# Kernel optimization log

Measured on AMD Instinct MI355X. Metric: run time of the kernel, lower is better.

Reference implementation:

```python
import jax, jax.numpy as jnp
import numpy as np
import math

NEG = -1e9


def maximum_path(neg_cent, text_len, spec_len):
    # neg_cent: [B, Ts, Tt]; monotonic alignment (Viterbi) DP as in VITS.
    B, Ts, Tt = neg_cent.shape
    jj = jnp.arange(Tt)
    tt = jnp.arange(Ts)
    node_mask = (jj[None, None, :] < text_len[:, None, None]) & (tt[None, :, None] < spec_len[:, None, None])
    nc = jnp.where(node_mask, neg_cent, NEG)

    def fstep(q, nc_t):
        # q: [B, Tt] best score ending at text index j at previous frame
        q_shift = jnp.concatenate([jnp.full((B, 1), NEG, q.dtype), q[:, :-1]], axis=1)
        d = q_shift >= q  # True -> came from j-1 (diagonal move)
        q_new = nc_t + jnp.maximum(q, q_shift)
        return q_new, d

    q0 = jnp.broadcast_to(jnp.where(jj == 0, 0.0, NEG), (B, Tt)).astype(neg_cent.dtype)
    _, dirs = jax.lax.scan(fstep, q0, jnp.swapaxes(nc, 0, 1))  # dirs: [Ts, B, Tt]

    def bstep(j, inp):
        t, d_t = inp
        start = (t == spec_len - 1)
        j_eff = jnp.where(start, text_len - 1, j)
        valid = t < spec_len
        emit = ((jj[None, :] == j_eff[:, None]) & valid[:, None]).astype(neg_cent.dtype)
        came_diag = jnp.take_along_axis(d_t, j_eff[:, None], axis=1)[:, 0]
        j_next = jnp.where(valid, jnp.maximum(j_eff - came_diag.astype(j_eff.dtype), 0), j_eff)
        return j_next, emit

    j_init = jnp.zeros((B,), text_len.dtype)
    _, path = jax.lax.scan(bstep, j_init, (jnp.arange(Ts), dirs), reverse=True)
    return jnp.swapaxes(path, 0, 1)  # [B, Ts, Tt]


def setup_inputs() -> dict:
    B, C, Ts, Tt = 16, 192, 2048, 512
    key = jax.random.key(0)
    k1, k2, k3, k4, k5 = jax.random.split(key, 5)
    z_p = jax.random.normal(k1, (B, C, Ts), dtype=jnp.float32)
    m_p = jax.random.normal(k2, (B, C, Tt), dtype=jnp.float32)
    logs_p = 0.1 * jax.random.normal(k3, (B, C, Tt), dtype=jnp.float32)
    text_len = jax.random.randint(k4, (B,), Tt // 2, Tt + 1, dtype=jnp.int32)
    extra = jax.random.randint(k5, (B,), 0, Ts - Tt + 1, dtype=jnp.int32)
    spec_len = jnp.minimum(text_len + extra, Ts)
    return {"z_p": z_p, "m_p": m_p, "logs_p": logs_p, "spec_len": spec_len, "text_len": text_len}


def reference(z_p, m_p, logs_p, spec_len, text_len):
    B, C, Ts = z_p.shape
    Tt = m_p.shape[2]
    text_mask = (jnp.arange(Tt)[None, :] < text_len[:, None]).astype(z_p.dtype)[:, None, :]  # [B,1,Tt]
    spec_mask = (jnp.arange(Ts)[None, :] < spec_len[:, None]).astype(z_p.dtype)[:, None, :]  # [B,1,Ts]

    # --- neg_cent (torch.no_grad block) ---
    s_p_sq_r = jnp.exp(-2.0 * logs_p)  # [B,C,Tt]
    neg_cent1 = jnp.sum(-0.5 * math.log(2.0 * math.pi) - logs_p, axis=1, keepdims=True)  # [B,1,Tt]
    neg_cent2 = jnp.einsum('bct,bcu->btu', -0.5 * z_p ** 2, s_p_sq_r)  # [B,Ts,Tt]
    neg_cent3 = jnp.einsum('bct,bcu->btu', z_p, m_p * s_p_sq_r)  # [B,Ts,Tt]
    neg_cent4 = jnp.sum(-0.5 * m_p ** 2 * s_p_sq_r, axis=1, keepdims=True)  # [B,1,Tt]
    neg_cent = neg_cent1 + neg_cent2 + neg_cent3 + neg_cent4

    path = jax.lax.stop_gradient(maximum_path(neg_cent, text_len, spec_len))  # [B,Ts,Tt]

    duration = jnp.sum(path, axis=1)[:, None, :]  # [B,1,Tt]
    logw_ = jnp.log(duration + 1e-6) * text_mask  # [B,1,Tt]

    # expand prior stats along the alignment path: [B,C,Ts]
    m_p_exp = jnp.einsum('btu,bcu->bct', path, m_p)
    logs_p_exp = jnp.einsum('btu,bcu->bct', path, logs_p)

    return (path, duration, logw_, m_p_exp, logs_p_exp, text_mask, spec_mask)
```

## Files before the change

kernel.cpp:

```cpp
#include <hip/hip_runtime.h>
#include <hip/hip_bf16.h>
#include <math.h>

#define BB 16
#define CC 192
#define TS 2048
#define TT 512
#define KK 384

#define OFF_PATH 0
#define OFF_DUR  (16777216)
#define OFF_LOGW (OFF_DUR + 8192)
#define OFF_MEXP (OFF_LOGW + 8192)
#define OFF_LEXP (OFF_MEXP + 6291456)
#define OFF_TMASK (OFF_LEXP + 6291456)
#define OFF_SMASK (OFF_TMASK + 8192)

#define NEGCF (-1e9f)

__global__ __launch_bounds__(512) void vits_prep(
    const float* __restrict__ m_p, const float* __restrict__ logs_p,
    const int* __restrict__ spec_len, const int* __restrict__ text_len,
    float* __restrict__ Bmat, float* __restrict__ avec,
    float* __restrict__ tmask, float* __restrict__ smask)
{
    const int b = blockIdx.x;
    const int u = threadIdx.x;
    const float C0 = -0.91893853320467274178f;
    float a_acc = 0.f;
    for (int c = 0; c < CC; ++c) {
        float lg = logs_p[((size_t)b*CC + c)*TT + u];
        float mm = m_p[((size_t)b*CC + c)*TT + u];
        float s  = expf(-2.f*lg);
        float ms = mm * s;
        Bmat[((size_t)b*KK + 2*c    )*TT + u] = ms;
        Bmat[((size_t)b*KK + 2*c + 1)*TT + u] = s;
        a_acc += C0 - lg - 0.5f*mm*ms;
    }
    avec[b*TT + u] = a_acc;
    tmask[b*TT + u] = (u < text_len[b]) ? 1.f : 0.f;
    for (int t = u; t < TS; t += TT)
        smask[b*TS + t] = (t < spec_len[b]) ? 1.f : 0.f;
}

__global__ __launch_bounds__(256) void vits_gemm(
    const float* __restrict__ z, const float* __restrict__ Bmat,
    const float* __restrict__ avec, float* __restrict__ out)
{
    const int b  = blockIdx.z;
    const int t0 = blockIdx.y * 64;
    const int u0 = blockIdx.x * 64;
    __shared__ float As[16][68];
    __shared__ float Bs[16][68];
    const int tid = threadIdx.x;
    const int tx = tid & 15, ty = tid >> 4;
    float acc[4][4] = {};
    const float* zb = z    + (size_t)b * CC * TS;
    const float* Bb = Bmat + (size_t)b * KK * TT;
    for (int kc = 0; kc < KK/16; ++kc) {
        {
            int c_l = tid >> 5;
            int t_l = (tid & 31) * 2;
            const float* zp = zb + (size_t)(kc*8 + c_l)*TS + t0 + t_l;
            float2 zv = *(const float2*)zp;
            float2 z1 = make_float2(zv.x, zv.y);
            float2 z2 = make_float2(-0.5f*zv.x*zv.x, -0.5f*zv.y*zv.y);
            *(float2*)&As[2*c_l  ][t_l] = z1;
            *(float2*)&As[2*c_l+1][t_l] = z2;
            int k_l = tid >> 4;
            int u_l = (tid & 15) * 4;
            const float* bp = Bb + (size_t)(kc*16 + k_l)*TT + u0 + u_l;
            *(float4*)&Bs[k_l][u_l] = *(const float4*)bp;
        }
        __syncthreads();
        #pragma unroll
        for (int kk = 0; kk < 16; ++kk) {
            float4 av = *(const float4*)&As[kk][ty*4];
            float4 bv = *(const float4*)&Bs[kk][tx*4];
            float aa[4] = {av.x, av.y, av.z, av.w};
            float bb[4] = {bv.x, bv.y, bv.z, bv.w};
            #pragma unroll
            for (int i = 0; i < 4; ++i)
                #pragma unroll
                for (int jj = 0; jj < 4; ++jj)
                    acc[i][jj] += aa[i]*bb[jj];
        }
        __syncthreads();
    }
    float4 a4 = *(const float4*)(avec + b*TT + u0 + tx*4);
    float ab[4] = {a4.x, a4.y, a4.z, a4.w};
    #pragma unroll
    for (int i = 0; i < 4; ++i) {
        float4 o;
        o.x = acc[i][0] + ab[0];
        o.y = acc[i][1] + ab[1];
        o.z = acc[i][2] + ab[2];
        o.w = acc[i][3] + ab[3];
        *(float4*)(out + ((size_t)b*TS + t0 + ty*4 + i)*TT + u0 + tx*4) = o;
    }
}

__device__ __forceinline__ float dpp_ror1_f32(float v) {
    union { float f; int i; } u, r;
    u.f = v;
    r.i = __builtin_amdgcn_update_dpp(0, u.i, 0x13C, 0xF, 0xF, false);
    return r.f;
}

#define DIRS(j,w) dirs[((j)<<6) | ((w) ^ ((j) & 31))]
#define RING 16

__global__ __launch_bounds__(1024, 1) void vits_dp(
    const float* __restrict__ nc,
    const int* __restrict__ spec_len, const int* __restrict__ text_len,
    float* __restrict__ dur, float* __restrict__ logw, int* __restrict__ jt)
{
    __shared__ unsigned int dirs[TT*(TS/32)];
    __shared__ float qrow[TT];
    __shared__ int Tr[TT + 1];

    const int tid  = threadIdx.x;
    const int lane = tid & 63;
    const int wid  = tid >> 6;
    const int b = blockIdx.x;
    const int SL = spec_len[b], TL = text_len[b];
    const int col = (wid << 5) + lane - 32;
    const bool auth = (lane >= 32);
    const bool w0g  = (wid == 0) && (lane < 32);

    float q = (col == 0) ? 0.0f : NEGCF;
    unsigned int bits = 0;

    const int colL = (col < 0) ? 0 : col;
    const float* ncb = nc + (size_t)b*TS*TT + colL;

    float pf[RING];
    #pragma unroll
    for (int i = 0; i < RING; ++i) pf[i] = ncb[(size_t)i*TT];
    const float* pcur = ncb + (size_t)RING*TT;

    int tb = 0;
    for (; tb + 32 <= SL; tb += 32) {
        #pragma unroll
        for (int s = 0; s < 32; ++s) {
            const int t = tb + s;
            float f = pf[s & (RING-1)];
            pf[s & (RING-1)] = *pcur;
            pcur += TT;

            float qp = dpp_ror1_f32(q);
            bool d = (qp >= q);
            bits = (bits << 1) | (unsigned)d;
            float qn = f + fmaxf(qp, q);
            q = w0g ? NEGCF : qn;

            if (s == 31) {
                int w = t >> 5;
                if (auth) {
                    DIRS(col, w) = bits;
                    qrow[col] = q;
                }
                bits = 0;
                __syncthreads();
                if (!auth && wid != 0) q = qrow[col];
                __syncthreads();
            }
        }
    }
    for (int t = tb; t < SL; ++t) {
        float f = ncb[(size_t)t*TT];
        float qp = dpp_ror1_f32(q);
        bool d = (qp >= q);
        bits = (bits << 1) | (unsigned)d;
        float qn = f + fmaxf(qp, q);
        q = w0g ? NEGCF : qn;
    }
    if (SL & 31) {
        int w = SL >> 5, r = SL & 31;
        if (auth) DIRS(col, w) = bits << (32 - r);
    }
    __syncthreads();

    for (int i = tid; i <= TT; i += 1024) Tr[i] = 0;
    __syncthreads();

    if (tid == 0) {
        Tr[TL] = SL;
        int j = TL - 1, tc = SL - 1;
        while (j > 0 && tc >= 0) {
            int w = tc >> 5;
            int bcur = 31 - (tc & 31);
            unsigned int W = DIRS(j, w) & (0xFFFFFFFFu << bcur);
            if (W) {
                int bp = __ffs(W) - 1;
                int tp = (w << 5) + 31 - bp;
                Tr[j] = tp;
                --j;
                tc = tp - 1;
            } else {
                if (w == 0) break;
                tc = (w << 5) - 1;
            }
        }
    }
    __syncthreads();

    for (int u = tid; u < TT; u += 1024) {
        float dv = (u < TL) ? (float)(Tr[u+1] - Tr[u]) : 0.0f;
        dur[b*TT + u] = dv;
        logw[b*TT + u] = (u < TL) ? logf(dv + 1e-6f) : 0.0f;
    }
    for (int u = 0; u < TL; ++u) {
        int t1 = Tr[u+1];
        for (int t = Tr[u] + tid; t < t1; t += 1024) jt[b*TS + t] = u;
    }
    for (int t = SL + tid; t < TS; t += 1024) jt[b*TS + t] = -1;
}

__global__ void vits_path(const int* __restrict__ jt, float4* __restrict__ path)
{
    int idx = blockIdx.x*blockDim.x + threadIdx.x;
    const int total = BB*TS*(TT/4);
    for (; idx < total; idx += gridDim.x*blockDim.x) {
        int u4 = idx & (TT/4 - 1);
        int bt = idx >> 7;
        int j = jt[bt];
        float4 v = make_float4(0.f,0.f,0.f,0.f);
        int r = j - (u4 << 2);
        if (r >= 0 && r < 4) ((float*)&v)[r] = 1.f;
        path[idx] = v;
    }
}

__global__ void vits_mlexp(const int* __restrict__ jt,
    const float* __restrict__ m_p, const float* __restrict__ logs_p,
    float4* __restrict__ mexp, float4* __restrict__ lexp)
{
    int idx = blockIdx.x*blockDim.x + threadIdx.x;
    const int total = BB*CC*(TS/4);
    for (; idx < total; idx += gridDim.x*blockDim.x) {
        int t4 = idx & (TS/4 - 1);
        int bc = idx >> 9;
        int b = bc / CC;
        int4 jv = *(const int4*)(jt + b*TS + (t4 << 2));
        const float* mrow = m_p    + (size_t)bc*TT;
        const float* lrow = logs_p + (size_t)bc*TT;
        float4 mv, lv;
        mv.x = (jv.x >= 0) ? mrow[jv.x] : 0.f;  lv.x = (jv.x >= 0) ? lrow[jv.x] : 0.f;
        mv.y = (jv.y >= 0) ? mrow[jv.y] : 0.f;  lv.y = (jv.y >= 0) ? lrow[jv.y] : 0.f;
        mv.z = (jv.z >= 0) ? mrow[jv.z] : 0.f;  lv.z = (jv.z >= 0) ? lrow[jv.z] : 0.f;
        mv.w = (jv.w >= 0) ? mrow[jv.w] : 0.f;  lv.w = (jv.w >= 0) ? lrow[jv.w] : 0.f;
        mexp[idx] = mv;
        lexp[idx] = lv;
    }
}

extern "C" void kernel_launch(void* const* d_in, const int* in_sizes, int n_in,
                              void* d_out, int out_size, void* d_ws, size_t ws_size,
                              hipStream_t stream) {
    const float* z_p      = (const float*)d_in[0];
    const float* m_p      = (const float*)d_in[1];
    const float* logs_p   = (const float*)d_in[2];
    const int*   spec_len = (const int*)d_in[3];
    const int*   text_len = (const int*)d_in[4];
    float* out = (float*)d_out;

    float* Bmat = (float*)d_ws;
    float* avec = Bmat + (size_t)BB*KK*TT;
    int*   jt   = (int*)(avec + BB*TT);

    float* path  = out + OFF_PATH;
    float* dur   = out + OFF_DUR;
    float* logw  = out + OFF_LOGW;
    float* mexp  = out + OFF_MEXP;
    float* lexp  = out + OFF_LEXP;
    float* tmask = out + OFF_TMASK;
    float* smask = out + OFF_SMASK;

    vits_prep<<<BB, 512, 0, stream>>>(m_p, logs_p, spec_len, text_len,
                                      Bmat, avec, tmask, smask);
    vits_gemm<<<dim3(TT/64, TS/64, BB), 256, 0, stream>>>(z_p, Bmat, avec, path);
    vits_dp<<<BB, 1024, 0, stream>>>(path, spec_len, text_len, dur, logw, jt);
    vits_path<<<2048, 256, 0, stream>>>(jt, (float4*)path);
    vits_mlexp<<<2048, 256, 0, stream>>>(jt, m_p, logs_p, (float4*)mexp, (float4*)lexp);
}
```

Baseline: 480.3 us.

## Stage DP rows into LDS with async double-buffered loads and shorter sync chunks

The forward Viterbi loop no longer uses a 16-deep register prefetch ring of global loads. Each chunk of 6 time rows is now staged into a double-buffered shared-memory area with global_load_lds, issued by 12 waves, and read from LDS. The halo exchange between waves now happens after every 6-row chunk through a double-buffered qrow array with one barrier, instead of two barriers every 32 rows. The aim is to take global load latency off the serial dependency chain, at the cost of many more barriers. There is also a possible race, because the loop has no explicit vmcnt wait before it reads the next staged buffer.

```diff
diff --git a/kernel.cpp b/kernel.cpp
--- a/kernel.cpp
+++ b/kernel.cpp
@@ -108,7 +108,7 @@
 }
 
 #define DIRS(j,w) dirs[((j)<<6) | ((w) ^ ((j) & 31))]
-#define RING 16
+#define CH 6
 
 __global__ __launch_bounds__(1024, 1) void vits_dp(
     const float* __restrict__ nc,
@@ -116,7 +116,8 @@
     float* __restrict__ dur, float* __restrict__ logw, int* __restrict__ jt)
 {
     __shared__ unsigned int dirs[TT*(TS/32)];
-    __shared__ float qrow[TT];
+    __shared__ float stg[2][CH*TT];
+    __shared__ float qrow2[2][TT];
     __shared__ int Tr[TT + 1];
 
     const int tid  = threadIdx.x;
@@ -127,53 +128,64 @@
     const int col = (wid << 5) + lane - 32;
     const bool auth = (lane >= 32);
     const bool w0g  = (wid == 0) && (lane < 32);
+    const int colL = (col < 0) ? 0 : col;
 
     float q = (col == 0) ? 0.0f : NEGCF;
     unsigned int bits = 0;
 
-    const int colL = (col < 0) ? 0 : col;
-    const float* ncb = nc + (size_t)b*TS*TT + colL;
-
-    float pf[RING];
-    #pragma unroll
-    for (int i = 0; i < RING; ++i) pf[i] = ncb[(size_t)i*TT];
-    const float* pcur = ncb + (size_t)RING*TT;
-
-    int tb = 0;
-    for (; tb + 32 <= SL; tb += 32) {
+    const float* ncb = nc + (size_t)b*TS*TT;
+
+    const int sr = wid >> 1, sh = wid & 1;
+    const int nch = SL / CH;
+
+    #define STAGE(cnext) do { \
+        if (wid < 2*CH) { \
+            int ts_ = (cnext)*CH + sr; if (ts_ > SL-1) ts_ = SL-1; \
+            const float* src_ = ncb + (size_t)ts_*TT + sh*256 + (lane << 2); \
+            __builtin_amdgcn_global_load_lds( \
+                (const __attribute__((address_space(1))) unsigned int*)src_, \
+                (__attribute__((address_space(3))) unsigned int*)&stg[(cnext)&1][sr*TT + sh*256], \
+                16, 0, 0); \
+        } } while (0)
+
+    STAGE(0);
+    asm volatile("s_waitcnt vmcnt(0)");
+    __syncthreads();
+
+    for (int c = 0; c < nch; ++c) {
+        STAGE(c+1);
+        const float* lrow = &stg[c & 1][colL];
+        float fr[CH];
         #pragma unroll
-        for (int s = 0; s < 32; ++s) {
-            const int t = tb + s;
-            float f = pf[s & (RING-1)];
-            pf[s & (RING-1)] = *pcur;
-            pcur += TT;
-
+        for (int r = 0; r < CH; ++r) fr[r] = lrow[r*TT];
+        #pragma unroll
+        for (int r = 0; r < CH; ++r) {
+            const int t = c*CH + r;
             float qp = dpp_ror1_f32(q);
             bool d = (qp >= q);
             bits = (bits << 1) | (unsigned)d;
-            float qn = f + fmaxf(qp, q);
+            float qn = fr[r] + fmaxf(qp, q);
             q = w0g ? NEGCF : qn;
-
-            if (s == 31) {
-                int w = t >> 5;
-                if (auth) {
-                    DIRS(col, w) = bits;
-                    qrow[col] = q;
-                }
+            if ((t & 31) == 31) {
+                if (auth) DIRS(col, t >> 5) = bits;
                 bits = 0;
-                __syncthreads();
-                if (!auth && wid != 0) q = qrow[col];
-                __syncthreads();
             }
         }
-    }
-    for (int t = tb; t < SL; ++t) {
-        float f = ncb[(size_t)t*TT];
+        if (auth) qrow2[c & 1][col] = q;
+        __syncthreads();
+        if (!auth && wid) q = qrow2[c & 1][col];
+    }
+    for (int t = nch*CH; t < SL; ++t) {
+        float f = ncb[(size_t)t*TT + colL];
         float qp = dpp_ror1_f32(q);
         bool d = (qp >= q);
         bits = (bits << 1) | (unsigned)d;
         float qn = f + fmaxf(qp, q);
         q = w0g ? NEGCF : qn;
+        if ((t & 31) == 31) {
+            if (auth) DIRS(col, t >> 5) = bits;
+            bits = 0;
+        }
     }
     if (SL & 31) {
         int w = SL >> 5, r = SL & 31;
```

Result: slower. 606.1 us (+26.2%).

## Interleave neg_cent by time groups of four and double-buffer DP prefetch

Applied to the files above, without the earlier changes.

The GEMM now writes neg_cent in a layout where four consecutive time steps for each text column sit together, so the DP kernel can fetch them with one float4 load instead of four strided scalar loads. The DP loop is restructured into 32-step phases with two register buffers: the next 32 steps are loaded while the current ones are computed. A double-buffered qrow array lets one __syncthreads per phase replace two. This raises register use for the prefetch buffers and changes the intermediate layout that both kernels must agree on.

```diff
diff --git a/kernel.cpp b/kernel.cpp
--- a/kernel.cpp
+++ b/kernel.cpp
@@ -17,6 +17,7 @@
 #define OFF_SMASK (OFF_TMASK + 8192)
 
 #define NEGCF (-1e9f)
+#define GSTR (TT*4)
 
 __global__ __launch_bounds__(512) void vits_prep(
     const float* __restrict__ m_p, const float* __restrict__ logs_p,
@@ -45,7 +46,7 @@
 
 __global__ __launch_bounds__(256) void vits_gemm(
     const float* __restrict__ z, const float* __restrict__ Bmat,
-    const float* __restrict__ avec, float* __restrict__ out)
+    const float* __restrict__ avec, float* __restrict__ ncT)
 {
     const int b  = blockIdx.z;
     const int t0 = blockIdx.y * 64;
@@ -89,14 +90,16 @@
     }
     float4 a4 = *(const float4*)(avec + b*TT + u0 + tx*4);
     float ab[4] = {a4.x, a4.y, a4.z, a4.w};
+    const int g = (t0 >> 2) + ty;
+    float* outp = ncT + (((size_t)b*(TS/4) + g)*TT + u0 + tx*4) * 4;
     #pragma unroll
-    for (int i = 0; i < 4; ++i) {
+    for (int jj = 0; jj < 4; ++jj) {
         float4 o;
-        o.x = acc[i][0] + ab[0];
-        o.y = acc[i][1] + ab[1];
-        o.z = acc[i][2] + ab[2];
-        o.w = acc[i][3] + ab[3];
-        *(float4*)(out + ((size_t)b*TS + t0 + ty*4 + i)*TT + u0 + tx*4) = o;
+        o.x = acc[0][jj] + ab[jj];
+        o.y = acc[1][jj] + ab[jj];
+        o.z = acc[2][jj] + ab[jj];
+        o.w = acc[3][jj] + ab[jj];
+        *(float4*)(outp + jj*4) = o;
     }
 }
 
@@ -108,15 +111,14 @@
 }
 
 #define DIRS(j,w) dirs[((j)<<6) | ((w) ^ ((j) & 31))]
-#define RING 16
 
 __global__ __launch_bounds__(1024, 1) void vits_dp(
-    const float* __restrict__ nc,
+    const float* __restrict__ ncT,
     const int* __restrict__ spec_len, const int* __restrict__ text_len,
     float* __restrict__ dur, float* __restrict__ logw, int* __restrict__ jt)
 {
     __shared__ unsigned int dirs[TT*(TS/32)];
-    __shared__ float qrow[TT];
+    __shared__ float qrow2[2][TT];
     __shared__ int Tr[TT + 1];
 
     const int tid  = threadIdx.x;
@@ -127,48 +129,50 @@
     const int col = (wid << 5) + lane - 32;
     const bool auth = (lane >= 32);
     const bool w0g  = (wid == 0) && (lane < 32);
+    const int colL = (col < 0) ? 0 : col;
 
     float q = (col == 0) ? 0.0f : NEGCF;
     unsigned int bits = 0;
 
-    const int colL = (col < 0) ? 0 : col;
-    const float* ncb = nc + (size_t)b*TS*TT + colL;
-
-    float pf[RING];
+    const float* base = ncT + (size_t)b*(TS/4)*GSTR + (size_t)colL*4;
+
+    float4 bufA[8], bufB[8];
     #pragma unroll
-    for (int i = 0; i < RING; ++i) pf[i] = ncb[(size_t)i*TT];
-    const float* pcur = ncb + (size_t)RING*TT;
+    for (int i = 0; i < 8; ++i) bufA[i] = *(const float4*)(base + (size_t)i*GSTR);
+
+#define PHASE(BUF, OBUF, PAR) do {                                           \
+        const int tn4 = (tb + 32) >> 2;                                      \
+        _Pragma("unroll")                                                    \
+        for (int i = 0; i < 8; ++i) {                                        \
+            int gi = tn4 + i; if (gi > TS/4 - 1) gi = TS/4 - 1;              \
+            OBUF[i] = *(const float4*)(base + (size_t)gi*GSTR);              \
+        }                                                                    \
+        _Pragma("unroll")                                                    \
+        for (int g4 = 0; g4 < 8; ++g4) {                                     \
+            _Pragma("unroll")                                                \
+            for (int k = 0; k < 4; ++k) {                                    \
+                float f = ((const float*)&BUF[g4])[k];                       \
+                float qp = dpp_ror1_f32(q);                                  \
+                bool d = (qp >= q);                                          \
+                bits = (bits << 1) | (unsigned)d;                            \
+                float qn = f + fmaxf(qp, q);                                 \
+                q = w0g ? NEGCF : qn;                                        \
+            }                                                                \
+        }                                                                    \
+        if (auth) { DIRS(col, tb >> 5) = bits; qrow2[PAR][col] = q; }        \
+        bits = 0;                                                            \
+        __syncthreads();                                                     \
+        if (!auth && wid) q = qrow2[PAR][col];                               \
+    } while (0)
 
     int tb = 0;
-    for (; tb + 32 <= SL; tb += 32) {
-        #pragma unroll
-        for (int s = 0; s < 32; ++s) {
-            const int t = tb + s;
-            float f = pf[s & (RING-1)];
-            pf[s & (RING-1)] = *pcur;
-            pcur += TT;
-
-            float qp = dpp_ror1_f32(q);
-            bool d = (qp >= q);
-            bits = (bits << 1) | (unsigned)d;
-            float qn = f + fmaxf(qp, q);
-            q = w0g ? NEGCF : qn;
-
-            if (s == 31) {
-                int w = t >> 5;
-                if (auth) {
-                    DIRS(col, w) = bits;
-                    qrow[col] = q;
-                }
-                bits = 0;
-                __syncthreads();
-                if (!auth && wid != 0) q = qrow[col];
-                __syncthreads();
-            }
-        }
+    const int nblk = SL >> 5;
+    for (int blk = 0; blk < nblk; ++blk, tb += 32) {
+        if ((blk & 1) == 0) PHASE(bufA, bufB, 0);
+        else                PHASE(bufB, bufA, 1);
     }
     for (int t = tb; t < SL; ++t) {
-        float f = ncb[(size_t)t*TT];
+        float f = base[((size_t)(t >> 2))*GSTR + (t & 3)];
         float qp = dpp_ror1_f32(q);
         bool d = (qp >= q);
         bits = (bits << 1) | (unsigned)d;
```

Result: slower. 659.3 us (+37.3%).
